# Optimization experiments

Hardware: AMD Instinct MI355X
Metric: run time of the kernel (lower is better)

Reference implementation:

```python
import jax, jax.numpy as jnp
import numpy as np

H = 32        # num_attention_heads
KVH = 8       # num_key_value_heads
D = 64        # attention_head_size
WIN = 256     # attention_window_size (left/right)
ROPE_BASE = 10000.0


def setup_inputs() -> dict:
    key = jax.random.key(0)
    k1, k2, k3 = jax.random.split(key, 3)
    B, S = 2, 2048
    return {
        "query_states": jax.random.normal(k1, (B, S, H * D), dtype=jnp.float32),
        "key_states": jax.random.normal(k2, (B, S, KVH * D), dtype=jnp.float32),
        "value_states": jax.random.normal(k3, (B, S, KVH * D), dtype=jnp.float32),
    }


def _rope_cos_sin(seq_len, dtype):
    inv_freq = 1.0 / (ROPE_BASE ** (jnp.arange(0, D, 2, dtype=jnp.float32) / D))  # [D/2]
    pos = jnp.arange(seq_len, dtype=jnp.float32)
    freqs = pos[:, None] * inv_freq[None, :]          # [S, D/2]
    emb = jnp.concatenate([freqs, freqs], axis=-1)    # [S, D]
    return jnp.cos(emb).astype(dtype), jnp.sin(emb).astype(dtype)


def _rotate_half(x):
    x1, x2 = x[..., : D // 2], x[..., D // 2 :]
    return jnp.concatenate([-x2, x1], axis=-1)


def reference(query_states, key_states, value_states):
    B, S, _ = query_states.shape
    n_rep = H // KVH

    q = query_states.reshape(B, S, H, D).transpose(0, 2, 1, 3)        # [B,H,S,D]
    k = key_states.reshape(B, S, KVH, D).transpose(0, 2, 1, 3)        # [B,KVH,S,D]
    v = value_states.reshape(B, S, KVH, D).transpose(0, 2, 1, 3)

    # repeat_kv: [B,KVH,S,D] -> [B,H,S,D]
    k = jnp.repeat(k, n_rep, axis=1)
    v = jnp.repeat(v, n_rep, axis=1)

    cos, sin = _rope_cos_sin(S, q.dtype)   # [S,D]
    cos = cos[None, None]                  # [1,1,S,D]
    sin = sin[None, None]
    q = q * cos + _rotate_half(q) * sin
    k = k * cos + _rotate_half(k) * sin

    scale = 1.0 / jnp.sqrt(jnp.asarray(D, dtype=q.dtype))
    scores = jnp.einsum("bhqd,bhkd->bhqk", q, k) * scale              # [B,H,S,S]

    i = jnp.arange(S)[:, None]
    j = jnp.arange(S)[None, :]
    allowed = (j >= i - WIN) & (j <= i)                               # [S,S]
    scores = jnp.where(allowed[None, None], scores, jnp.finfo(scores.dtype).min)

    probs = jax.nn.softmax(scores, axis=-1)
    out = jnp.einsum("bhqk,bhkd->bhqd", probs, v)                     # [B,H,S,D]
    return out.transpose(0, 2, 1, 3).reshape(B, S, H * D)
```

## Files before the change

kernel.cpp:

```cpp
#include <hip/hip_runtime.h>
#include <math.h>

#define NH   32
#define NKVH 8
#define HD   64
#define WIN  256
#define BB   2
#define SS   2048

typedef short short8 __attribute__((ext_vector_type(8)));
typedef float f32x4  __attribute__((ext_vector_type(4)));

__device__ __forceinline__ ushort f2bf(float x) {
    union { float f; unsigned u; } v; v.f = x;
    unsigned u = v.u + 0x7FFF + ((v.u >> 16) & 1);
    return (ushort)(u >> 16);
}

__device__ __forceinline__ int cvtpk_bf16(float lo, float hi) {
    int r;
    asm("v_cvt_pk_bf16_f32 %0, %1, %2" : "=v"(r) : "v"(lo), "v"(hi));
    return r;
}

__device__ __forceinline__ int swz(int L) { return L ^ (((L >> 7) & 7) << 4); }

__device__ __forceinline__ void stage16(const void* g, void* l) {
    __builtin_amdgcn_global_load_lds(
        (const __attribute__((address_space(1))) unsigned int*)g,
        (__attribute__((address_space(3))) unsigned int*)l, 16, 0, 0);
}

__global__ __launch_bounds__(256) void prep_kv(const float* __restrict__ K,
                                               const float* __restrict__ V,
                                               ushort* __restrict__ Kr,
                                               ushort* __restrict__ Vt) {
    __shared__ __align__(16) ushort ldsK[2048];
    __shared__ __align__(16) ushort ldsV[2048];
    const int bidx = blockIdx.x;
    const int sblk = bidx & 63;
    const int s0   = sblk * 32;
    const int kvh  = (bidx >> 6) & 7;
    const int b    = bidx >> 9;
    const int tid  = threadIdx.x;

    {
        const int key = tid >> 3, dg = tid & 7;
        const int s   = s0 + key;
        const float* krow = K + (size_t)(b * SS + s) * (NKVH * HD) + kvh * HD + dg * 8;
        float x[8];
        *(float4*)(x)     = *(const float4*)(krow);
        *(float4*)(x + 4) = *(const float4*)(krow + 4);
        float inv = __powf(10000.f, -(float)((dg & 3) * 8) * (1.f / 32.f));
        const float ratio = 0.74989420933f;
        ushort out[8];
#pragma unroll
        for (int j = 0; j < 8; ++j) {
            float partner = __shfl(x[j], (tid & 63) ^ 4, 64);
            float sn, cs;
            __sincosf((float)s * inv, &sn, &cs);
            out[j] = f2bf(x[j] * cs + ((dg < 4) ? -partner : partner) * sn);
            inv *= ratio;
        }
        *(short8*)((char*)ldsK + swz(key * 128 + dg * 16)) = *(short8*)out;
    }
    {
        const int kp = tid & 15, dq = tid >> 4;
        const int c  = 2 * kp;
        const int kf = ((c >> 3) * 4) + (c & 3) + (((c >> 2) & 1) * 16);
        const float* v0 = V + (size_t)(b * SS + s0 + kf) * (NKVH * HD) + kvh * HD + dq * 4;
        float4 a = *(const float4*)v0;
        float4 cvec = *(const float4*)(v0 + NKVH * HD);
#pragma unroll
        for (int j = 0; j < 4; ++j) {
            int d = dq * 4 + j;
            unsigned w = (unsigned)f2bf(((const float*)&a)[j])
                       | ((unsigned)f2bf(((const float*)&cvec)[j]) << 16);
            *(unsigned*)((char*)ldsV + swz(d * 64 + kp * 4)) = w;
        }
    }
    __syncthreads();
    char* kc = (char*)(Kr + (size_t)(b * NKVH + kvh) * SS * HD) + (size_t)sblk * 4096;
    char* vc = (char*)(Vt + (size_t)(b * NKVH + kvh) * HD * SS) + (size_t)sblk * 4096;
    *(short8*)(kc + tid * 16) = *(short8*)((char*)ldsK + tid * 16);
    *(short8*)(vc + tid * 16) = *(short8*)((char*)ldsV + tid * 16);
}

__global__ __launch_bounds__(256, 4) void attn_mfma(const float* __restrict__ Q,
                                                    const ushort* __restrict__ Kr,
                                                    const ushort* __restrict__ Vt,
                                                    float* __restrict__ O) {
    __shared__ __align__(16) ushort ldsK[2][2][2048];
    __shared__ __align__(16) ushort ldsV[2][2][2048];
    const int wv = threadIdx.x >> 6, lane = threadIdx.x & 63;
    const int lo16 = lane & 15, quad = lane >> 4;
    const int bidx = (blockIdx.x & 7) * 128 + (blockIdx.x >> 3);
    const int qblk = bidx & 63;
    const int kvh  = (bidx >> 6) & 7;
    const int b    = bidx >> 9;
    const int h    = kvh * 4 + wv;
    const int q0   = qblk * 32;

    float invf[8];
#pragma unroll
    for (int j = 0; j < 8; ++j)
        invf[j] = __powf(10000.f, -(float)(quad * 8 + j) * (1.f / 32.f));

    short8 aq[2][2];
#pragma unroll
    for (int t = 0; t < 2; ++t) {
        int qi = q0 + t * 16 + lo16;
        const float* qrow = Q + (size_t)(b * SS + qi) * (NH * HD) + h * HD;
        float lo[8], hi[8];
        *(float4*)(lo)     = *(const float4*)(qrow + quad * 8);
        *(float4*)(lo + 4) = *(const float4*)(qrow + quad * 8 + 4);
        *(float4*)(hi)     = *(const float4*)(qrow + 32 + quad * 8);
        *(float4*)(hi + 4) = *(const float4*)(qrow + 32 + quad * 8 + 4);
#pragma unroll
        for (int j = 0; j < 8; ++j) {
            float sn, cs;
            __sincosf((float)qi * invf[j], &sn, &cs);
            aq[t][0][j] = (short)f2bf((lo[j] * cs - hi[j] * sn) * 0.125f);
            aq[t][1][j] = (short)f2bf((hi[j] * cs + lo[j] * sn) * 0.125f);
        }
    }

    const char* kbase = (const char*)(Kr + (size_t)(b * NKVH + kvh) * SS * HD);
    const char* vbase = (const char*)(Vt + (size_t)(b * NKVH + kvh) * HD * SS);

    f32x4 acc[2][4];
#pragma unroll
    for (int t = 0; t < 2; ++t)
#pragma unroll
        for (int i = 0; i < 4; ++i) acc[t][i] = (f32x4){0.f, 0.f, 0.f, 0.f};
    float psum[2] = {0.f, 0.f};

    int klo = q0 - WIN; if (klo < 0) klo = 0;
    const int c0  = klo >> 5;
    const int cnt = (q0 >> 5) - c0 + 1;
    const int npairs = (cnt + 1) >> 1;

    auto stagepair = [&](int pidx, int buf) {
        int ca = c0 + 2 * pidx, cb = ca + 1;
        if (ca > SS / 32 - 1) ca = SS / 32 - 1;
        if (cb > SS / 32 - 1) cb = SS / 32 - 1;
        stage16(kbase + (size_t)ca * 4096 + wv * 1024 + lane * 16,
                (char*)&ldsK[buf][0][0] + wv * 1024);
        stage16(vbase + (size_t)ca * 4096 + wv * 1024 + lane * 16,
                (char*)&ldsV[buf][0][0] + wv * 1024);
        stage16(kbase + (size_t)cb * 4096 + wv * 1024 + lane * 16,
                (char*)&ldsK[buf][1][0] + wv * 1024);
        stage16(vbase + (size_t)cb * 4096 + wv * 1024 + lane * 16,
                (char*)&ldsV[buf][1][0] + wv * 1024);
    };

    auto compute = [&](int kb, const char* kl, const char* vl) {
        short8 k0 = *(const short8*)(kl + swz(lo16 * 128 + quad * 16));
        short8 k1 = *(const short8*)(kl + swz(lo16 * 128 + 64 + quad * 16));
        short8 k2 = *(const short8*)(kl + swz((lo16 + 16) * 128 + quad * 16));
        short8 k3 = *(const short8*)(kl + swz((lo16 + 16) * 128 + 64 + quad * 16));

        const f32x4 z = {0.f, 0.f, 0.f, 0.f};
        __builtin_amdgcn_s_setprio(1);
        f32x4 s00 = __builtin_amdgcn_mfma_f32_16x16x32_bf16(k0, aq[0][0], z,   0, 0, 0);
        s00       = __builtin_amdgcn_mfma_f32_16x16x32_bf16(k1, aq[0][1], s00, 0, 0, 0);
        f32x4 s01 = __builtin_amdgcn_mfma_f32_16x16x32_bf16(k2, aq[0][0], z,   0, 0, 0);
        s01       = __builtin_amdgcn_mfma_f32_16x16x32_bf16(k3, aq[0][1], s01, 0, 0, 0);
        f32x4 s10 = __builtin_amdgcn_mfma_f32_16x16x32_bf16(k0, aq[1][0], z,   0, 0, 0);
        s10       = __builtin_amdgcn_mfma_f32_16x16x32_bf16(k1, aq[1][1], s10, 0, 0, 0);
        f32x4 s11 = __builtin_amdgcn_mfma_f32_16x16x32_bf16(k2, aq[1][0], z,   0, 0, 0);
        s11       = __builtin_amdgcn_mfma_f32_16x16x32_bf16(k3, aq[1][1], s11, 0, 0, 0);
        __builtin_amdgcn_s_setprio(0);

        short8 ap[2];
#pragma unroll
        for (int t = 0; t < 2; ++t) {
            const f32x4 sa = t ? s10 : s00;
            const f32x4 sb = t ? s11 : s01;
            const int qtmin = q0 + t * 16;
            const int myq   = qtmin + lo16;
            float p[8];
            if ((kb + 31 > qtmin) || (kb < qtmin + 15 - WIN)) {
#pragma unroll
                for (int r = 0; r < 4; ++r) {
                    int key0 = kb + quad * 4 + r;
                    int key1 = key0 + 16;
                    p[r]     = (key0 <= myq && key0 >= myq - WIN) ? __expf(sa[r]) : 0.f;
                    p[4 + r] = (key1 <= myq && key1 >= myq - WIN) ? __expf(sb[r]) : 0.f;
                }
            } else {
#pragma unroll
                for (int r = 0; r < 4; ++r) { p[r] = __expf(sa[r]); p[4 + r] = __expf(sb[r]); }
            }
            psum[t] += ((p[0] + p[1]) + (p[2] + p[3])) + ((p[4] + p[5]) + (p[6] + p[7]));

            union { int i[4]; short8 s; } u;
            u.i[0] = cvtpk_bf16(p[0], p[1]);
            u.i[1] = cvtpk_bf16(p[2], p[3]);
            u.i[2] = cvtpk_bf16(p[4], p[5]);
            u.i[3] = cvtpk_bf16(p[6], p[7]);
            ap[t] = u.s;
        }

        short8 vf[4];
#pragma unroll
        for (int i = 0; i < 4; ++i)
            vf[i] = *(const short8*)(vl + swz((i * 16 + lo16) * 64 + quad * 16));

        __builtin_amdgcn_s_setprio(1);
#pragma unroll
        for (int i = 0; i < 4; ++i)
            acc[0][i] = __builtin_amdgcn_mfma_f32_16x16x32_bf16(ap[0], vf[i], acc[0][i], 0, 0, 0);
#pragma unroll
        for (int i = 0; i < 4; ++i)
            acc[1][i] = __builtin_amdgcn_mfma_f32_16x16x32_bf16(ap[1], vf[i], acc[1][i], 0, 0, 0);
        __builtin_amdgcn_s_setprio(0);
    };

    stagepair(0, 0);

    int nb = 0;
    for (int p = 0; p < npairs; ++p, nb ^= 1) {
        stagepair(p + 1, nb ^ 1);
        asm volatile("s_waitcnt vmcnt(4)" ::: "memory");
        __builtin_amdgcn_s_barrier();
        __builtin_amdgcn_sched_barrier(0);
        compute(klo + 2 * p * 32, (const char*)&ldsK[nb][0][0], (const char*)&ldsV[nb][0][0]);
        if (2 * p + 1 < cnt)
            compute(klo + (2 * p + 1) * 32, (const char*)&ldsK[nb][1][0], (const char*)&ldsV[nb][1][0]);
        __builtin_amdgcn_sched_barrier(0);
        __builtin_amdgcn_s_barrier();
    }

#pragma unroll
    for (int t = 0; t < 2; ++t) {
        float ps = psum[t];
        ps += __shfl_xor(ps, 16, 64);
        ps += __shfl_xor(ps, 32, 64);
#pragma unroll
        for (int r = 0; r < 4; ++r) {
            float invr = 1.f / __shfl(ps, quad * 4 + r, 16);
            int qr = q0 + t * 16 + quad * 4 + r;
            size_t orow = ((size_t)(b * SS + qr) * NH + h) * HD;
            O[orow + 0 * 16 + lo16] = acc[t][0][r] * invr;
            O[orow + 1 * 16 + lo16] = acc[t][1][r] * invr;
            O[orow + 2 * 16 + lo16] = acc[t][2][r] * invr;
            O[orow + 3 * 16 + lo16] = acc[t][3][r] * invr;
        }
    }
}

__device__ __forceinline__ float wave_sum(float x) {
#pragma unroll
    for (int off = 32; off > 0; off >>= 1) x += __shfl_xor(x, off, 64);
    return x;
}

__global__ __launch_bounds__(256) void attn_scalar(const float* __restrict__ Q,
                                                   const float* __restrict__ K,
                                                   const float* __restrict__ V,
                                                   float* __restrict__ O) {
    int wave = blockIdx.x * 4 + (threadIdx.x >> 6);
    int lane = threadIdx.x & 63;
    int q  = wave % SS;
    int bh = wave / SS;
    int h  = bh % NH;
    int b  = bh / NH;
    int kvh = h >> 2;

    float inv = __powf(10000.f, -(float)(lane & 31) * (1.f / 32.f));
    float sn, cs;
    __sincosf((float)q * inv, &sn, &cs);

    float qv = Q[(size_t)(b * SS + q) * (NH * HD) + h * HD + lane];
    float qpart = __shfl(qv, lane ^ 32, 64);
    float qrot = (qv * cs + ((lane < 32) ? -qpart : qpart) * sn) * 0.125f;

    const float* vbase = V + (size_t)b * SS * (NKVH * HD) + kvh * HD;
    float m = -1e30f, l = 0.f, acc = 0.f;
    int k0 = q - WIN; if (k0 < 0) k0 = 0;
    for (int k = k0; k <= q; ++k) {
        float kraw = K[(size_t)(b * SS + k) * (NKVH * HD) + kvh * HD + lane];
        float kpart = __shfl(kraw, lane ^ 32, 64);
        float ksn, kcs;
        __sincosf((float)k * inv, &ksn, &kcs);
        float kv = kraw * kcs + ((lane < 32) ? -kpart : kpart) * ksn;
        float vv = vbase[(size_t)k * (NKVH * HD) + lane];
        float score = wave_sum(qrot * kv);
        float mnew  = fmaxf(m, score);
        float alpha = __expf(m - mnew);
        float p     = __expf(score - mnew);
        l   = l * alpha + p;
        acc = acc * alpha + p * vv;
        m   = mnew;
    }
    O[(((size_t)(b * SS + q) * NH) + h) * HD + lane] = acc / l;
}

extern "C" void kernel_launch(void* const* d_in, const int* in_sizes, int n_in,
                              void* d_out, int out_size, void* d_ws, size_t ws_size,
                              hipStream_t stream) {
    const float* Q = (const float*)d_in[0];
    const float* K = (const float*)d_in[1];
    const float* V = (const float*)d_in[2];
    float* O = (float*)d_out;

    size_t kv_elems = (size_t)BB * NKVH * SS * HD;
    size_t need = 2 * kv_elems * sizeof(ushort);

    if (ws_size >= need) {
        ushort* Kr = (ushort*)d_ws;
        ushort* Vt = Kr + kv_elems;
        prep_kv<<<BB * NKVH * (SS / 32), 256, 0, stream>>>(K, V, Kr, Vt);
        attn_mfma<<<BB * NKVH * (SS / 32), 256, 0, stream>>>(Q, Kr, Vt, O);
    } else {
        attn_scalar<<<(BB * NH * SS) / 4, 256, 0, stream>>>(Q, K, V, O);
    }
}
```

Before: 113.1 us.

## Process two query blocks per workgroup sharing staged K/V tiles

```diff
diff --git a/kernel.cpp b/kernel.cpp
--- a/kernel.cpp
+++ b/kernel.cpp
@@ -86,20 +86,21 @@
     *(short8*)(vc + tid * 16) = *(short8*)((char*)ldsV + tid * 16);
 }
 
-__global__ __launch_bounds__(256, 4) void attn_mfma(const float* __restrict__ Q,
+__global__ __launch_bounds__(512, 4) void attn_mfma(const float* __restrict__ Q,
                                                     const ushort* __restrict__ Kr,
                                                     const ushort* __restrict__ Vt,
                                                     float* __restrict__ O) {
     __shared__ __align__(16) ushort ldsK[2][2][2048];
     __shared__ __align__(16) ushort ldsV[2][2][2048];
-    const int wv = threadIdx.x >> 6, lane = threadIdx.x & 63;
+    const int tid = threadIdx.x;
+    const int wv = tid >> 6, lane = tid & 63;
     const int lo16 = lane & 15, quad = lane >> 4;
-    const int bidx = (blockIdx.x & 7) * 128 + (blockIdx.x >> 3);
-    const int qblk = bidx & 63;
-    const int kvh  = (bidx >> 6) & 7;
-    const int b    = bidx >> 9;
-    const int h    = kvh * 4 + wv;
-    const int q0   = qblk * 32;
+    const int bidx  = (blockIdx.x & 7) * 64 + (blockIdx.x >> 3);
+    const int qpair = bidx & 31;
+    const int kvh   = (bidx >> 5) & 7;
+    const int b     = bidx >> 8;
+    const int h     = kvh * 4 + (wv & 3);
+    const int q0    = qpair * 64 + (wv >> 2) * 32;
 
     float invf[8];
 #pragma unroll
@@ -135,23 +136,25 @@
         for (int i = 0; i < 4; ++i) acc[t][i] = (f32x4){0.f, 0.f, 0.f, 0.f};
     float psum[2] = {0.f, 0.f};
 
-    int klo = q0 - WIN; if (klo < 0) klo = 0;
-    const int c0  = klo >> 5;
-    const int cnt = (q0 >> 5) - c0 + 1;
-    const int npairs = (cnt + 1) >> 1;
+    int klo = qpair * 64 - WIN; if (klo < 0) klo = 0;
+    const int c0     = klo >> 5;
+    const int cnt    = 2 * qpair + 2 - c0;
+    const int npairs = cnt >> 1;
 
     auto stagepair = [&](int pidx, int buf) {
-        int ca = c0 + 2 * pidx, cb = ca + 1;
-        if (ca > SS / 32 - 1) ca = SS / 32 - 1;
-        if (cb > SS / 32 - 1) cb = SS / 32 - 1;
-        stage16(kbase + (size_t)ca * 4096 + wv * 1024 + lane * 16,
-                (char*)&ldsK[buf][0][0] + wv * 1024);
-        stage16(vbase + (size_t)ca * 4096 + wv * 1024 + lane * 16,
-                (char*)&ldsV[buf][0][0] + wv * 1024);
-        stage16(kbase + (size_t)cb * 4096 + wv * 1024 + lane * 16,
-                (char*)&ldsK[buf][1][0] + wv * 1024);
-        stage16(vbase + (size_t)cb * 4096 + wv * 1024 + lane * 16,
-                (char*)&ldsV[buf][1][0] + wv * 1024);
+        const int ca = c0 + 2 * pidx, cb = ca + 1;
+        const int im   = wv >> 1;
+        const int hoff = (wv & 1) * 2048;
+        const char* src = (im == 0) ? kbase + (size_t)ca * 4096
+                        : (im == 1) ? vbase + (size_t)ca * 4096
+                        : (im == 2) ? kbase + (size_t)cb * 4096
+                        :             vbase + (size_t)cb * 4096;
+        char* dst = (im == 0) ? (char*)&ldsK[buf][0][0]
+                  : (im == 1) ? (char*)&ldsV[buf][0][0]
+                  : (im == 2) ? (char*)&ldsK[buf][1][0]
+                  :             (char*)&ldsV[buf][1][0];
+        stage16(src + hoff + lane * 16,        dst + hoff);
+        stage16(src + hoff + 1024 + lane * 16, dst + hoff + 1024);
     };
 
     auto compute = [&](int kb, const char* kl, const char* vl) {
@@ -221,13 +224,16 @@
 
     int nb = 0;
     for (int p = 0; p < npairs; ++p, nb ^= 1) {
-        stagepair(p + 1, nb ^ 1);
-        asm volatile("s_waitcnt vmcnt(4)" ::: "memory");
+        if (p + 1 < npairs) {
+            stagepair(p + 1, nb ^ 1);
+            asm volatile("s_waitcnt vmcnt(2)" ::: "memory");
+        } else {
+            asm volatile("s_waitcnt vmcnt(0)" ::: "memory");
+        }
         __builtin_amdgcn_s_barrier();
         __builtin_amdgcn_sched_barrier(0);
-        compute(klo + 2 * p * 32, (const char*)&ldsK[nb][0][0], (const char*)&ldsV[nb][0][0]);
-        if (2 * p + 1 < cnt)
-            compute(klo + (2 * p + 1) * 32, (const char*)&ldsK[nb][1][0], (const char*)&ldsV[nb][1][0]);
+        compute(klo + 2 * p * 32,       (const char*)&ldsK[nb][0][0], (const char*)&ldsV[nb][0][0]);
+        compute(klo + (2 * p + 1) * 32, (const char*)&ldsK[nb][1][0], (const char*)&ldsV[nb][1][0]);
         __builtin_amdgcn_sched_barrier(0);
         __builtin_amdgcn_s_barrier();
     }
@@ -312,7 +318,7 @@
         ushort* Kr = (ushort*)d_ws;
         ushort* Vt = Kr + kv_elems;
         prep_kv<<<BB * NKVH * (SS / 32), 256, 0, stream>>>(K, V, Kr, Vt);
-        attn_mfma<<<BB * NKVH * (SS / 32), 256, 0, stream>>>(Q, Kr, Vt, O);
+        attn_mfma<<<BB * NKVH * (SS / 64), 512, 0, stream>>>(Q, Kr, Vt, O);
     } else {
         attn_scalar<<<(BB * NH * SS) / 4, 256, 0, stream>>>(Q, K, V, O);
     }
```

After: 115.0 us. Within noise of the previous version (+1.7%).

## Replace pairwise double-buffered K/V staging with 5-slot ring, 3-deep prefetch

Applied to the files above, without the earlier changes.

```diff
diff --git a/kernel.cpp b/kernel.cpp
--- a/kernel.cpp
+++ b/kernel.cpp
@@ -90,8 +90,8 @@
                                                     const ushort* __restrict__ Kr,
                                                     const ushort* __restrict__ Vt,
                                                     float* __restrict__ O) {
-    __shared__ __align__(16) ushort ldsK[2][2][2048];
-    __shared__ __align__(16) ushort ldsV[2][2][2048];
+    __shared__ __align__(16) ushort ldsK[5][2048];
+    __shared__ __align__(16) ushort ldsV[5][2048];
     const int wv = threadIdx.x >> 6, lane = threadIdx.x & 63;
     const int lo16 = lane & 15, quad = lane >> 4;
     const int bidx = (blockIdx.x & 7) * 128 + (blockIdx.x >> 3);
@@ -138,20 +138,14 @@
     int klo = q0 - WIN; if (klo < 0) klo = 0;
     const int c0  = klo >> 5;
     const int cnt = (q0 >> 5) - c0 + 1;
-    const int npairs = (cnt + 1) >> 1;
-
-    auto stagepair = [&](int pidx, int buf) {
-        int ca = c0 + 2 * pidx, cb = ca + 1;
-        if (ca > SS / 32 - 1) ca = SS / 32 - 1;
-        if (cb > SS / 32 - 1) cb = SS / 32 - 1;
-        stage16(kbase + (size_t)ca * 4096 + wv * 1024 + lane * 16,
-                (char*)&ldsK[buf][0][0] + wv * 1024);
-        stage16(vbase + (size_t)ca * 4096 + wv * 1024 + lane * 16,
-                (char*)&ldsV[buf][0][0] + wv * 1024);
-        stage16(kbase + (size_t)cb * 4096 + wv * 1024 + lane * 16,
-                (char*)&ldsK[buf][1][0] + wv * 1024);
-        stage16(vbase + (size_t)cb * 4096 + wv * 1024 + lane * 16,
-                (char*)&ldsV[buf][1][0] + wv * 1024);
+    const int clast = c0 + cnt - 1;
+
+    auto stagechunk = [&](int cidx, int slot) {
+        if (cidx > clast) cidx = clast;
+        stage16(kbase + (size_t)cidx * 4096 + wv * 1024 + lane * 16,
+                (char*)&ldsK[slot][0] + wv * 1024);
+        stage16(vbase + (size_t)cidx * 4096 + wv * 1024 + lane * 16,
+                (char*)&ldsV[slot][0] + wv * 1024);
     };
 
     auto compute = [&](int kb, const char* kl, const char* vl) {
@@ -217,19 +211,16 @@
         __builtin_amdgcn_s_setprio(0);
     };
 
-    stagepair(0, 0);
-
-    int nb = 0;
-    for (int p = 0; p < npairs; ++p, nb ^= 1) {
-        stagepair(p + 1, nb ^ 1);
-        asm volatile("s_waitcnt vmcnt(4)" ::: "memory");
+    stagechunk(c0,     0);
+    stagechunk(c0 + 1, 1);
+    stagechunk(c0 + 2, 2);
+
+    for (int i = 0; i < cnt; ++i) {
+        stagechunk(c0 + i + 3, (i + 3) % 5);
+        asm volatile("s_waitcnt vmcnt(6)" ::: "memory");
         __builtin_amdgcn_s_barrier();
         __builtin_amdgcn_sched_barrier(0);
-        compute(klo + 2 * p * 32, (const char*)&ldsK[nb][0][0], (const char*)&ldsV[nb][0][0]);
-        if (2 * p + 1 < cnt)
-            compute(klo + (2 * p + 1) * 32, (const char*)&ldsK[nb][1][0], (const char*)&ldsV[nb][1][0]);
-        __builtin_amdgcn_sched_barrier(0);
-        __builtin_amdgcn_s_barrier();
+        compute(klo + i * 32, (const char*)&ldsK[i % 5][0], (const char*)&ldsV[i % 5][0]);
     }
 
 #pragma unroll
```

After: 113.2 us. No clear change (+0.1%).
